# Optimization experiments

Hardware: AMD Instinct MI355X
Metric: run time of the kernel (lower is better)

The kernel has to match this reference:

```python
import jax, jax.numpy as jnp
import numpy as np

K = 16          # neighbors per query (args.k)
EPS_NORM = 1e-5  # LayerNorm / BatchNorm eps (torch default)


def _knn_edges(xyz, B, n):
    # batch-aware kNN: equal-sized batches, edges never cross batch boundary
    x = xyz.reshape(B, n, 3)
    d2 = jnp.sum((x[:, :, None, :] - x[:, None, :, :]) ** 2, -1)   # [B,n,n]
    _, idx = jax.lax.top_k(-d2, K)                                 # [B,n,K] local neighbor ids
    col = (idx + (jnp.arange(B) * n)[:, None, None]).reshape(-1)   # source (neighbor) [E]
    row = jnp.repeat(jnp.arange(B * n), K)                         # target (query)    [E]
    return row, col


def _forward(support_xyz, batch_index, features, lang_features, mask_flattened,
             W1, b1, ln_g, ln_b, W2, b2,
             Wl1, bl1, bn_g, bn_b, Wl2, bl2,
             Wr1, br1, Wr2, br2, row, col):
    N = support_xyz.shape[0]
    B, L, Fl = lang_features.shape
    # feat_encoder: Linear -> LayerNorm -> ReLU -> Linear
    h = features @ W1 + b1
    mu = h.mean(-1, keepdims=True)
    var = ((h - mu) ** 2).mean(-1, keepdims=True)
    h = (h - mu) / jnp.sqrt(var + EPS_NORM) * ln_g + ln_b
    feats = jax.nn.relu(h) @ W2 + b2                               # [N,F]
    # lang_encoder: Linear -> BatchNorm1d (batch statistics) -> ReLU -> Linear
    hl = lang_features.reshape(B * L, Fl) @ Wl1 + bl1
    mul = hl.mean(0)
    varl = ((hl - mul) ** 2).mean(0)
    hl = (hl - mul) / jnp.sqrt(varl + EPS_NORM) * bn_g + bn_b
    lang = (jax.nn.relu(hl) @ Wl2 + bl2).reshape(B, L, -1)         # [B,L,F]
    lang_flat = lang[batch_index]                                  # [N,L,F]
    # per-point / per-token attention logits
    atten = jnp.einsum('nf,nlf->nl', feats, lang_flat)             # [N,L]
    # segment softmax over incoming kNN edges (CenterOp max / add)
    attenmax = jax.ops.segment_max(atten[col], row, num_segments=N, indices_are_sorted=True)
    a = jnp.exp(atten[col] - attenmax[row])                        # [E,L]
    attensum = jax.ops.segment_sum(a, row, num_segments=N, indices_are_sorted=True)
    # CenterConv message
    att = a / attensum[row] * mask_flattened[row]                  # [E,L]
    att = att / (att.sum(-1, keepdims=True) + 1e-7)
    ctx = jnp.einsum('el,elf->ef', att, lang_flat[col])            # [E,F] attended lang feat
    xi, xj = support_xyz[row], support_xyz[col]
    d = xi - xj
    nrm = jnp.sqrt(jnp.sum(d * d, -1, keepdims=True) + 1e-12)
    ew = jnp.concatenate([xi, xj, d, nrm], -1)                     # [E,10]
    ew = jax.nn.relu(ew @ Wr1 + br1) @ Wr2 + br2                   # [E,F] rel_encoder
    msg = feats[col] * ctx * ew                                    # [E,F]
    rel = jax.ops.segment_sum(msg, row, num_segments=N, indices_are_sorted=True)
    return feats + rel


def setup_inputs() -> dict:
    key = jax.random.key(0)
    ks = jax.random.split(key, 12)
    B, n, L = 4, 1024, 16
    N = B * n
    Fv, Fl, F = 256, 768, 128
    def w(k, shp, fan):
        return jax.random.normal(k, shp, jnp.float32) / np.sqrt(fan).astype(np.float32)
    mask = (jax.random.uniform(ks[3], (N, L)) < 0.8).astype(jnp.float32).at[:, 0].set(1.0)
    return {
        'support_xyz': jax.random.normal(ks[0], (N, 3), jnp.float32),
        'batch_index': jnp.repeat(jnp.arange(B), n),
        'features': jax.random.normal(ks[1], (N, Fv), jnp.float32),
        'lang_features': jax.random.normal(ks[2], (B, L, Fl), jnp.float32),
        'mask_flattened': mask,
        'W1': w(ks[4], (Fv, F), Fv), 'b1': jnp.zeros(F, jnp.float32),
        'ln_g': jnp.ones(F, jnp.float32), 'ln_b': jnp.zeros(F, jnp.float32),
        'W2': w(ks[5], (F, F), F), 'b2': jnp.zeros(F, jnp.float32),
        'Wl1': w(ks[6], (Fl, F), Fl), 'bl1': jnp.zeros(F, jnp.float32),
        'bn_g': jnp.ones(F, jnp.float32), 'bn_b': jnp.zeros(F, jnp.float32),
        'Wl2': w(ks[7], (F, F), F), 'bl2': jnp.zeros(F, jnp.float32),
        'Wr1': w(ks[8], (10, 64), 10), 'br1': jnp.zeros(64, jnp.float32),
        'Wr2': w(ks[9], (64, F), 64), 'br2': jnp.zeros(F, jnp.float32),
    }


def reference(support_xyz, batch_index, features, lang_features, mask_flattened,
              W1, b1, ln_g, ln_b, W2, b2,
              Wl1, bl1, bn_g, bn_b, Wl2, bl2,
              Wr1, br1, Wr2, br2):
    B = lang_features.shape[0]
    n = support_xyz.shape[0] // B
    row, col = _knn_edges(support_xyz, B, n)
    return _forward(support_xyz, batch_index, features, lang_features, mask_flattened,
                    W1, b1, ln_g, ln_b, W2, b2,
                    Wl1, bl1, bn_g, bn_b, Wl2, bl2,
                    Wr1, br1, Wr2, br2, row, col)
```

## Files before the change

### kernel.cpp

```cpp
#include <hip/hip_runtime.h>

typedef unsigned long long u64;
typedef short short8 __attribute__((ext_vector_type(8)));
typedef float f32x4 __attribute__((ext_vector_type(4)));

#define N_PTS   4096
#define B_SZ    4
#define N_PER_B 1024
#define L_TOK   16
#define FV      256
#define FL      768
#define FDIM    128
#define KNN     16
#define RH      64

__device__ __forceinline__ short f2bf(float f) {
    unsigned int x = __float_as_uint(f);
    unsigned int r = (x + 0x7fffu + ((x >> 16) & 1u)) >> 16;
    return (short)r;
}

__global__ __launch_bounds__(256) void k1_kernel(const float* __restrict__ xyz,
                                                 const float* __restrict__ features,
                                                 const float* __restrict__ lf,
                                                 const float* __restrict__ W1,
                                                 const float* __restrict__ b1,
                                                 const float* __restrict__ ln_g,
                                                 const float* __restrict__ ln_b,
                                                 const float* __restrict__ W2,
                                                 const float* __restrict__ b2,
                                                 const float* __restrict__ Wl1,
                                                 const float* __restrict__ bl1,
                                                 int* __restrict__ knn,
                                                 float* __restrict__ feats,
                                                 float* __restrict__ hl) {
    __shared__ float smem[4 * 256 + 4 * 128 + 16];
    int b = blockIdx.x, t = threadIdx.x;

    if (b < 1024) {
        int lane = t & 63;
        int q = b * 4 + (t >> 6);
        int base = (q >> 10) << 10;
        float qx = xyz[q * 3 + 0];
        float qy = xyz[q * 3 + 1];
        float qz = xyz[q * 3 + 2];
        u64 keys[16];
#pragma unroll
        for (int m = 0; m < 16; m++) {
            int j = base + lane + (m << 6);
            float dx = qx - xyz[j * 3 + 0];
            float dy = qy - xyz[j * 3 + 1];
            float dz = qz - xyz[j * 3 + 2];
            float d2 = __fadd_rn(__fadd_rn(__fmul_rn(dx, dx), __fmul_rn(dy, dy)),
                                 __fmul_rn(dz, dz));
            keys[m] = (((u64)__float_as_uint(d2)) << 32) | (unsigned int)j;
        }
        for (int r = 0; r < KNN; r++) {
            u64 lmin = keys[0];
#pragma unroll
            for (int m = 1; m < 16; m++) lmin = (keys[m] < lmin) ? keys[m] : lmin;
            u64 g = lmin;
#pragma unroll
            for (int off = 32; off > 0; off >>= 1) {
                u64 o = __shfl_xor(g, off, 64);
                g = (o < g) ? o : g;
            }
#pragma unroll
            for (int m = 0; m < 16; m++)
                if (keys[m] == g) keys[m] = ~0ULL;
            if (lane == 0) knn[q * KNN + r] = (int)(g & 0xffffffffu);
        }
    } else if (b < 2048) {
        int i0 = (b - 1024) * 4;
        float* fin  = smem;
        float* rbuf = smem + 1024;
        float* red  = smem + 1536;
        for (int p = t; p < 4 * FV; p += 256) {
            int pp = p >> 8, k = p & 255;
            fin[pp * FV + k] = features[(i0 + pp) * FV + k];
        }
        __syncthreads();
        int c = t & 127, h = t >> 7;
        int p0 = 2 * h, p1 = 2 * h + 1;
        float bv = b1[c];
        float acc0 = bv, acc1 = bv;
        for (int k = 0; k < FV; k++) {
            float w = W1[k * FDIM + c];
            acc0 += fin[p0 * FV + k] * w;
            acc1 += fin[p1 * FV + k] * w;
        }
        float s0 = acc0, q0 = acc0 * acc0, s1 = acc1, q1 = acc1 * acc1;
#pragma unroll
        for (int off = 32; off > 0; off >>= 1) {
            s0 += __shfl_xor(s0, off, 64);
            q0 += __shfl_xor(q0, off, 64);
            s1 += __shfl_xor(s1, off, 64);
            q1 += __shfl_xor(q1, off, 64);
        }
        int wid = t >> 6;
        if ((t & 63) == 0) {
            red[wid * 4 + 0] = s0; red[wid * 4 + 1] = q0;
            red[wid * 4 + 2] = s1; red[wid * 4 + 3] = q1;
        }
        __syncthreads();
        float S0 = red[(2 * h) * 4 + 0] + red[(2 * h + 1) * 4 + 0];
        float Q0 = red[(2 * h) * 4 + 1] + red[(2 * h + 1) * 4 + 1];
        float S1 = red[(2 * h) * 4 + 2] + red[(2 * h + 1) * 4 + 2];
        float Q1 = red[(2 * h) * 4 + 3] + red[(2 * h + 1) * 4 + 3];
        float g = ln_g[c], bb = ln_b[c];
        float mu0 = S0 * (1.f / 128.f), var0 = Q0 * (1.f / 128.f) - mu0 * mu0;
        float mu1 = S1 * (1.f / 128.f), var1 = Q1 * (1.f / 128.f) - mu1 * mu1;
        float r0 = fmaxf((acc0 - mu0) * rsqrtf(var0 + 1e-5f) * g + bb, 0.f);
        float r1 = fmaxf((acc1 - mu1) * rsqrtf(var1 + 1e-5f) * g + bb, 0.f);
        rbuf[p0 * FDIM + c] = r0;
        rbuf[p1 * FDIM + c] = r1;
        __syncthreads();
        float b2v = b2[c];
        float f0 = b2v, f1 = b2v;
        for (int k = 0; k < FDIM; k++) {
            float w = W2[k * FDIM + c];
            f0 += rbuf[p0 * FDIM + k] * w;
            f1 += rbuf[p1 * FDIM + k] * w;
        }
        feats[(i0 + p0) * FDIM + c] = f0;
        feats[(i0 + p1) * FDIM + c] = f1;
    } else {
        int r = b - 2048;
        float* lrow = smem;
        float* part = smem + 768;
        for (int k = t; k < FL; k += 256) lrow[k] = lf[r * FL + k];
        __syncthreads();
        int c = t & 127, kh = t >> 7;
        float acc = (kh == 0) ? bl1[c] : 0.f;
        int k0 = kh * 384;
        for (int k = k0; k < k0 + 384; k++) acc += lrow[k] * Wl1[k * FDIM + c];
        part[kh * FDIM + c] = acc;
        __syncthreads();
        if (kh == 0) hl[r * FDIM + c] = part[c] + part[FDIM + c];
    }
}

__global__ __launch_bounds__(128) void lang2_kernel(const float* __restrict__ hl,
                                                    const float* __restrict__ bn_g,
                                                    const float* __restrict__ bn_b,
                                                    const float* __restrict__ Wl2,
                                                    const float* __restrict__ bl2,
                                                    float* __restrict__ lang) {
    __shared__ float rl4[4][FDIM];
    int t = threadIdx.x;
    int r0 = blockIdx.x * 4;
    float s = 0.f, s2 = 0.f;
    for (int r = 0; r < 64; r++) {
        float v = hl[r * FDIM + t];
        s += v; s2 += v * v;
    }
    float mu = s * (1.f / 64.f);
    float var = s2 * (1.f / 64.f) - mu * mu;
    float rs = rsqrtf(var + 1e-5f);
    float g = bn_g[t], bb = bn_b[t];
#pragma unroll
    for (int p = 0; p < 4; p++)
        rl4[p][t] = fmaxf((hl[(r0 + p) * FDIM + t] - mu) * rs * g + bb, 0.f);
    __syncthreads();
    float bv = bl2[t];
    float a0 = bv, a1 = bv, a2 = bv, a3 = bv;
    for (int k = 0; k < FDIM; k++) {
        float w = Wl2[k * FDIM + t];
        a0 += rl4[0][k] * w;
        a1 += rl4[1][k] * w;
        a2 += rl4[2][k] * w;
        a3 += rl4[3][k] * w;
    }
    lang[(r0 + 0) * FDIM + t] = a0;
    lang[(r0 + 1) * FDIM + t] = a1;
    lang[(r0 + 2) * FDIM + t] = a2;
    lang[(r0 + 3) * FDIM + t] = a3;
}

__global__ __launch_bounds__(256) void atten_kernel(const float* __restrict__ feats,
                                                    const float* __restrict__ lang,
                                                    float* __restrict__ atten) {
    __shared__ float fb[2][FDIM];
    __shared__ float pb[256];
    int t = threadIdx.x;
    int half = t >> 7, tt = t & 127;
    int i = blockIdx.x * 2 + half;
    fb[half][tt] = feats[i * FDIM + tt];
    __syncthreads();
    int l = tt >> 3, sj = tt & 7;
    int bi = i >> 10;
    const float* lrow = lang + (bi * L_TOK + l) * FDIM;
    float p = 0.f;
#pragma unroll
    for (int m = 0; m < 16; m++) {
        int k = sj + (m << 3);
        p += fb[half][k] * lrow[k];
    }
    pb[t] = p;
    __syncthreads();
    if (tt < L_TOK) {
        float a = 0.f;
#pragma unroll
        for (int u = 0; u < 8; u++) a += pb[half * 128 + tt * 8 + u];
        atten[i * L_TOK + tt] = a;
    }
}

__global__ __launch_bounds__(256) void edge_kernel(const float* __restrict__ xyz,
                                                   const float* __restrict__ mask,
                                                   const float* __restrict__ Wr1,
                                                   const float* __restrict__ br1,
                                                   const float* __restrict__ Wr2,
                                                   const float* __restrict__ br2,
                                                   const int* __restrict__ knn,
                                                   const float* __restrict__ lang,
                                                   const float* __restrict__ feats,
                                                   const float* __restrict__ atten,
                                                   float* __restrict__ out) {
    int lane = threadIdx.x & 63;
    int wid  = threadIdx.x >> 6;
    int i    = blockIdx.x * 4 + wid;
    int bi   = i >> 10;
    int quad = lane >> 4;
    int e16  = lane & 15;

    int idxe = knn[i * KNN + e16];

    float sat[8];
    if (quad < 2) {
        const float4* ap = (const float4*)(atten + idxe * L_TOK + quad * 8);
        float4 a0 = ap[0], a1 = ap[1];
        sat[0] = a0.x; sat[1] = a0.y; sat[2] = a0.z; sat[3] = a0.w;
        sat[4] = a1.x; sat[5] = a1.y; sat[6] = a1.z; sat[7] = a1.w;
    } else {
#pragma unroll
        for (int j = 0; j < 8; j++) sat[j] = 0.f;
    }

    float mx[8];
#pragma unroll
    for (int j = 0; j < 8; j++) mx[j] = sat[j];
#pragma unroll
    for (int off = 1; off < 16; off <<= 1) {
#pragma unroll
        for (int j = 0; j < 8; j++) mx[j] = fmaxf(mx[j], __shfl_xor(mx[j], off, 16));
    }
    float ex[8], sm[8];
#pragma unroll
    for (int j = 0; j < 8; j++) { ex[j] = __expf(sat[j] - mx[j]); sm[j] = ex[j]; }
#pragma unroll
    for (int off = 1; off < 16; off <<= 1) {
#pragma unroll
        for (int j = 0; j < 8; j++) sm[j] += __shfl_xor(sm[j], off, 16);
    }
    float st[8];
    if (quad < 2) {
        const float4* mp = (const float4*)(mask + i * L_TOK + quad * 8);
        float4 m0 = mp[0], m1 = mp[1];
        float mv[8] = {m0.x, m0.y, m0.z, m0.w, m1.x, m1.y, m1.z, m1.w};
#pragma unroll
        for (int j = 0; j < 8; j++) st[j] = ex[j] * (mv[j] / sm[j]);
    } else {
#pragma unroll
        for (int j = 0; j < 8; j++) st[j] = 0.f;
    }
    float s = st[0] + st[1] + st[2] + st[3] + st[4] + st[5] + st[6] + st[7];
    s += __shfl_xor(s, 16, 64);
    s += __shfl_xor(s, 32, 64);
    float inv2 = 1.f / (s + 1e-7f);
    short8 sattA;
#pragma unroll
    for (int j = 0; j < 8; j++) sattA[j] = f2bf(st[j] * inv2);

    float xi0 = xyz[i * 3 + 0], xi1 = xyz[i * 3 + 1], xi2 = xyz[i * 3 + 2];
    float xj0 = xyz[idxe * 3 + 0], xj1 = xyz[idxe * 3 + 1], xj2 = xyz[idxe * 3 + 2];
    float d0 = xi0 - xj0, d1 = xi1 - xj1, d2v = xi2 - xj2;
    float nr = sqrtf(d0 * d0 + d1 * d1 + d2v * d2v + 1e-12f);
    float ein[10] = {xi0, xi1, xi2, xj0, xj1, xj2, d0, d1, d2v, nr};
    short8 hidA[2];
#pragma unroll
    for (int sstep = 0; sstep < 2; sstep++) {
        int k0 = sstep * 32 + quad * 8;
        float h[8];
        const float4* bp = (const float4*)(br1 + k0);
        float4 b0 = bp[0], b1v = bp[1];
        h[0] = b0.x; h[1] = b0.y; h[2] = b0.z; h[3] = b0.w;
        h[4] = b1v.x; h[5] = b1v.y; h[6] = b1v.z; h[7] = b1v.w;
#pragma unroll
        for (int m = 0; m < 10; m++) {
            const float4* wp = (const float4*)(Wr1 + m * RH + k0);
            float4 w0 = wp[0], w1 = wp[1];
            float em = ein[m];
            h[0] += em * w0.x; h[1] += em * w0.y; h[2] += em * w0.z; h[3] += em * w0.w;
            h[4] += em * w1.x; h[5] += em * w1.y; h[6] += em * w1.z; h[7] += em * w1.w;
        }
#pragma unroll
        for (int j = 0; j < 8; j++) hidA[sstep][j] = f2bf(fmaxf(h[j], 0.f));
    }

    int idxr[4];
#pragma unroll
    for (int r = 0; r < 4; r++) idxr[r] = knn[i * KNN + quad * 4 + r];

#pragma unroll 2
    for (int tile = 0; tile < 8; tile++) {
        int cc = tile * 16 + e16;
        f32x4 accew = {0.f, 0.f, 0.f, 0.f};
#pragma unroll
        for (int sstep = 0; sstep < 2; sstep++) {
            short8 w2B;
#pragma unroll
            for (int j = 0; j < 8; j++)
                w2B[j] = f2bf(Wr2[(sstep * 32 + quad * 8 + j) * FDIM + cc]);
            accew = __builtin_amdgcn_mfma_f32_16x16x32_bf16(hidA[sstep], w2B, accew, 0, 0, 0);
        }
        short8 lsB;
        if (quad < 2) {
#pragma unroll
            for (int j = 0; j < 8; j++)
                lsB[j] = f2bf(lang[bi * L_TOK * FDIM + (quad * 8 + j) * FDIM + cc]);
        } else {
#pragma unroll
            for (int j = 0; j < 8; j++) lsB[j] = 0;
        }
        f32x4 accctx = {0.f, 0.f, 0.f, 0.f};
        accctx = __builtin_amdgcn_mfma_f32_16x16x32_bf16(sattA, lsB, accctx, 0, 0, 0);

        float br2c = br2[cc];
        float msum = 0.f;
#pragma unroll
        for (int r = 0; r < 4; r++) {
            float fj = feats[idxr[r] * FDIM + cc];
            msum += fj * accctx[r] * (accew[r] + br2c);
        }
        msum += __shfl_xor(msum, 16, 64);
        msum += __shfl_xor(msum, 32, 64);
        if (lane < 16)
            out[i * FDIM + cc] = feats[i * FDIM + cc] + msum;
    }
}

extern "C" void kernel_launch(void* const* d_in, const int* in_sizes, int n_in,
                              void* d_out, int out_size, void* d_ws, size_t ws_size,
                              hipStream_t stream) {
    const float* xyz   = (const float*)d_in[0];
    const float* features = (const float*)d_in[2];
    const float* lang_f   = (const float*)d_in[3];
    const float* mask     = (const float*)d_in[4];
    const float* W1   = (const float*)d_in[5];
    const float* b1   = (const float*)d_in[6];
    const float* ln_g = (const float*)d_in[7];
    const float* ln_b = (const float*)d_in[8];
    const float* W2   = (const float*)d_in[9];
    const float* b2   = (const float*)d_in[10];
    const float* Wl1  = (const float*)d_in[11];
    const float* bl1  = (const float*)d_in[12];
    const float* bn_g = (const float*)d_in[13];
    const float* bn_b = (const float*)d_in[14];
    const float* Wl2  = (const float*)d_in[15];
    const float* bl2  = (const float*)d_in[16];
    const float* Wr1  = (const float*)d_in[17];
    const float* br1  = (const float*)d_in[18];
    const float* Wr2  = (const float*)d_in[19];
    const float* br2  = (const float*)d_in[20];

    float* ws_feats = (float*)d_ws;
    float* ws_atten = ws_feats + N_PTS * FDIM;
    float* ws_lang  = ws_atten + N_PTS * L_TOK;
    float* ws_hl    = ws_lang + B_SZ * L_TOK * FDIM;
    int*   ws_knn   = (int*)(ws_hl + 64 * FDIM);

    k1_kernel<<<2112, 256, 0, stream>>>(xyz, features, lang_f,
                                        W1, b1, ln_g, ln_b, W2, b2,
                                        Wl1, bl1, ws_knn, ws_feats, ws_hl);
    lang2_kernel<<<16, 128, 0, stream>>>(ws_hl, bn_g, bn_b, Wl2, bl2, ws_lang);
    atten_kernel<<<N_PTS / 2, 256, 0, stream>>>(ws_feats, ws_lang, ws_atten);
    edge_kernel<<<N_PTS / 4, 256, 0, stream>>>(xyz, mask, Wr1, br1, Wr2, br2,
                                               ws_knn, ws_lang, ws_feats, ws_atten,
                                               (float*)d_out);
}
```

Measured before the change: 166.0 us.

## Compute feat encoder with split-bf16 MFMA and fuse lang BN stage into new kernel

Result: no change. 164.1 us (-1.1%).

```diff
diff --git a/kernel.cpp b/kernel.cpp
--- a/kernel.cpp
+++ b/kernel.cpp
@@ -1,8 +1,10 @@
 #include <hip/hip_runtime.h>
 
 typedef unsigned long long u64;
+typedef unsigned int u32;
 typedef short short8 __attribute__((ext_vector_type(8)));
 typedef float f32x4 __attribute__((ext_vector_type(4)));
+typedef u32 u32x4v __attribute__((ext_vector_type(4)));
 
 #define N_PTS   4096
 #define B_SZ    4
@@ -14,6 +16,8 @@
 #define KNN     16
 #define RH      64
 
+#define MFMA_BF16(a, b, c) __builtin_amdgcn_mfma_f32_16x16x32_bf16((a), (b), (c), 0, 0, 0)
+
 __device__ __forceinline__ short f2bf(float f) {
     unsigned int x = __float_as_uint(f);
     unsigned int r = (x + 0x7fffu + ((x >> 16) & 1u)) >> 16;
@@ -23,18 +27,19 @@
 __global__ __launch_bounds__(256) void k1_kernel(const float* __restrict__ xyz,
                                                  const float* __restrict__ features,
                                                  const float* __restrict__ lf,
-                                                 const float* __restrict__ W1,
-                                                 const float* __restrict__ b1,
-                                                 const float* __restrict__ ln_g,
-                                                 const float* __restrict__ ln_b,
-                                                 const float* __restrict__ W2,
-                                                 const float* __restrict__ b2,
                                                  const float* __restrict__ Wl1,
                                                  const float* __restrict__ bl1,
+                                                 const float* __restrict__ W1,
+                                                 const float* __restrict__ W2,
                                                  int* __restrict__ knn,
-                                                 float* __restrict__ feats,
-                                                 float* __restrict__ hl) {
-    __shared__ float smem[4 * 256 + 4 * 128 + 16];
+                                                 float* __restrict__ hl,
+                                                 short* __restrict__ fp_hi,
+                                                 short* __restrict__ fp_lo,
+                                                 short* __restrict__ w1p_hi,
+                                                 short* __restrict__ w1p_lo,
+                                                 short* __restrict__ w2p_hi,
+                                                 short* __restrict__ w2p_lo) {
+    __shared__ float smem[1024];
     int b = blockIdx.x, t = threadIdx.x;
 
     if (b < 1024) {
@@ -70,62 +75,8 @@
                 if (keys[m] == g) keys[m] = ~0ULL;
             if (lane == 0) knn[q * KNN + r] = (int)(g & 0xffffffffu);
         }
-    } else if (b < 2048) {
-        int i0 = (b - 1024) * 4;
-        float* fin  = smem;
-        float* rbuf = smem + 1024;
-        float* red  = smem + 1536;
-        for (int p = t; p < 4 * FV; p += 256) {
-            int pp = p >> 8, k = p & 255;
-            fin[pp * FV + k] = features[(i0 + pp) * FV + k];
-        }
-        __syncthreads();
-        int c = t & 127, h = t >> 7;
-        int p0 = 2 * h, p1 = 2 * h + 1;
-        float bv = b1[c];
-        float acc0 = bv, acc1 = bv;
-        for (int k = 0; k < FV; k++) {
-            float w = W1[k * FDIM + c];
-            acc0 += fin[p0 * FV + k] * w;
-            acc1 += fin[p1 * FV + k] * w;
-        }
-        float s0 = acc0, q0 = acc0 * acc0, s1 = acc1, q1 = acc1 * acc1;
-#pragma unroll
-        for (int off = 32; off > 0; off >>= 1) {
-            s0 += __shfl_xor(s0, off, 64);
-            q0 += __shfl_xor(q0, off, 64);
-            s1 += __shfl_xor(s1, off, 64);
-            q1 += __shfl_xor(q1, off, 64);
-        }
-        int wid = t >> 6;
-        if ((t & 63) == 0) {
-            red[wid * 4 + 0] = s0; red[wid * 4 + 1] = q0;
-            red[wid * 4 + 2] = s1; red[wid * 4 + 3] = q1;
-        }
-        __syncthreads();
-        float S0 = red[(2 * h) * 4 + 0] + red[(2 * h + 1) * 4 + 0];
-        float Q0 = red[(2 * h) * 4 + 1] + red[(2 * h + 1) * 4 + 1];
-        float S1 = red[(2 * h) * 4 + 2] + red[(2 * h + 1) * 4 + 2];
-        float Q1 = red[(2 * h) * 4 + 3] + red[(2 * h + 1) * 4 + 3];
-        float g = ln_g[c], bb = ln_b[c];
-        float mu0 = S0 * (1.f / 128.f), var0 = Q0 * (1.f / 128.f) - mu0 * mu0;
-        float mu1 = S1 * (1.f / 128.f), var1 = Q1 * (1.f / 128.f) - mu1 * mu1;
-        float r0 = fmaxf((acc0 - mu0) * rsqrtf(var0 + 1e-5f) * g + bb, 0.f);
-        float r1 = fmaxf((acc1 - mu1) * rsqrtf(var1 + 1e-5f) * g + bb, 0.f);
-        rbuf[p0 * FDIM + c] = r0;
-        rbuf[p1 * FDIM + c] = r1;
-        __syncthreads();
-        float b2v = b2[c];
-        float f0 = b2v, f1 = b2v;
-        for (int k = 0; k < FDIM; k++) {
-            float w = W2[k * FDIM + c];
-            f0 += rbuf[p0 * FDIM + k] * w;
-            f1 += rbuf[p1 * FDIM + k] * w;
-        }
-        feats[(i0 + p0) * FDIM + c] = f0;
-        feats[(i0 + p1) * FDIM + c] = f1;
-    } else {
-        int r = b - 2048;
+    } else if (b < 1088) {
+        int r = b - 1024;
         float* lrow = smem;
         float* part = smem + 768;
         for (int k = t; k < FL; k += 256) lrow[k] = lf[r * FL + k];
@@ -137,44 +88,205 @@
         part[kh * FDIM + c] = acc;
         __syncthreads();
         if (kh == 0) hl[r * FDIM + c] = part[c] + part[FDIM + c];
+    } else if (b < 1344) {
+        int rt = b - 1088;
+        int lane = t & 63, kh = t >> 6;
+        int e = lane & 15, q = lane >> 4;
+#pragma unroll
+        for (int pp = 0; pp < 2; pp++) {
+            int ks = kh * 2 + pp;
+            const float* src = features + (rt * 16 + e) * FV + ks * 32 + q * 8;
+            float4 f0 = *(const float4*)src;
+            float4 f1 = *(const float4*)(src + 4);
+            float f[8] = {f0.x, f0.y, f0.z, f0.w, f1.x, f1.y, f1.z, f1.w};
+            short8 hi, lo;
+#pragma unroll
+            for (int j = 0; j < 8; j++) {
+                u32 bits = __float_as_uint(f[j]);
+                hi[j] = (short)(bits >> 16);
+                float lof = f[j] - __uint_as_float(bits & 0xffff0000u);
+                lo[j] = (short)(__float_as_uint(lof) >> 16);
+            }
+            int o = ((rt * 8 + ks) * 64 + lane) * 8;
+            *(short8*)(fp_hi + o) = hi;
+            *(short8*)(fp_lo + o) = lo;
+        }
+    } else {
+        int isW2 = (b >= 1352);
+        int ks = isW2 ? (b - 1352) : (b - 1344);
+        const float* W = isW2 ? W2 : W1;
+        short* ph = isW2 ? w2p_hi : w1p_hi;
+        short* pl = isW2 ? w2p_lo : w1p_lo;
+        int lane = t & 63, cth = t >> 6;
+        int e = lane & 15, q = lane >> 4;
+#pragma unroll
+        for (int p = 0; p < 2; p++) {
+            int ct = cth * 2 + p;
+            short8 hi, lo;
+#pragma unroll
+            for (int j = 0; j < 8; j++) {
+                float w = W[(ks * 32 + q * 8 + j) * FDIM + ct * 16 + e];
+                u32 bits = __float_as_uint(w);
+                hi[j] = (short)(bits >> 16);
+                float lof = w - __uint_as_float(bits & 0xffff0000u);
+                lo[j] = (short)(__float_as_uint(lof) >> 16);
+            }
+            int o = ((ks * 8 + ct) * 64 + lane) * 8;
+            *(short8*)(ph + o) = hi;
+            *(short8*)(pl + o) = lo;
+        }
     }
 }
 
-__global__ __launch_bounds__(128) void lang2_kernel(const float* __restrict__ hl,
-                                                    const float* __restrict__ bn_g,
-                                                    const float* __restrict__ bn_b,
-                                                    const float* __restrict__ Wl2,
-                                                    const float* __restrict__ bl2,
-                                                    float* __restrict__ lang) {
-    __shared__ float rl4[4][FDIM];
-    int t = threadIdx.x;
-    int r0 = blockIdx.x * 4;
-    float s = 0.f, s2 = 0.f;
-    for (int r = 0; r < 64; r++) {
-        float v = hl[r * FDIM + t];
-        s += v; s2 += v * v;
-    }
-    float mu = s * (1.f / 64.f);
-    float var = s2 * (1.f / 64.f) - mu * mu;
-    float rs = rsqrtf(var + 1e-5f);
-    float g = bn_g[t], bb = bn_b[t];
-#pragma unroll
-    for (int p = 0; p < 4; p++)
-        rl4[p][t] = fmaxf((hl[(r0 + p) * FDIM + t] - mu) * rs * g + bb, 0.f);
-    __syncthreads();
-    float bv = bl2[t];
-    float a0 = bv, a1 = bv, a2 = bv, a3 = bv;
-    for (int k = 0; k < FDIM; k++) {
-        float w = Wl2[k * FDIM + t];
-        a0 += rl4[0][k] * w;
-        a1 += rl4[1][k] * w;
-        a2 += rl4[2][k] * w;
-        a3 += rl4[3][k] * w;
-    }
-    lang[(r0 + 0) * FDIM + t] = a0;
-    lang[(r0 + 1) * FDIM + t] = a1;
-    lang[(r0 + 2) * FDIM + t] = a2;
-    lang[(r0 + 3) * FDIM + t] = a3;
+__global__ __launch_bounds__(256) void k2_kernel(const short* __restrict__ fp_hi,
+                                                 const short* __restrict__ fp_lo,
+                                                 const short* __restrict__ w1p_hi,
+                                                 const short* __restrict__ w1p_lo,
+                                                 const short* __restrict__ w2p_hi,
+                                                 const short* __restrict__ w2p_lo,
+                                                 const float* __restrict__ b1,
+                                                 const float* __restrict__ ln_g,
+                                                 const float* __restrict__ ln_b,
+                                                 const float* __restrict__ b2,
+                                                 const float* __restrict__ hl,
+                                                 const float* __restrict__ bn_g,
+                                                 const float* __restrict__ bn_b,
+                                                 const float* __restrict__ Wl2,
+                                                 const float* __restrict__ bl2,
+                                                 float* __restrict__ feats,
+                                                 float* __restrict__ lang) {
+    int b = blockIdx.x, t = threadIdx.x;
+    if (b < 64) {
+        __shared__ u32 hbuf[4][16 * 132];
+        int wid = t >> 6, lane = t & 63;
+        int e = lane & 15, q = lane >> 4;
+        int rt = b * 4 + wid;
+
+        f32x4 acc[8];
+#pragma unroll
+        for (int ct = 0; ct < 8; ct++) {
+            float v = b1[ct * 16 + e];
+            acc[ct] = (f32x4){v, v, v, v};
+        }
+        for (int ks = 0; ks < 8; ks++) {
+            int ao = ((rt * 8 + ks) * 64 + lane) * 8;
+            short8 ah = *(const short8*)(fp_hi + ao);
+            short8 al = *(const short8*)(fp_lo + ao);
+#pragma unroll
+            for (int ct = 0; ct < 8; ct++) {
+                int bo = ((ks * 8 + ct) * 64 + lane) * 8;
+                short8 bh = *(const short8*)(w1p_hi + bo);
+                short8 bl = *(const short8*)(w1p_lo + bo);
+                acc[ct] = MFMA_BF16(ah, bh, acc[ct]);
+                acc[ct] = MFMA_BF16(al, bh, acc[ct]);
+                acc[ct] = MFMA_BF16(ah, bl, acc[ct]);
+            }
+        }
+        float s[4], sq[4];
+#pragma unroll
+        for (int r = 0; r < 4; r++) { s[r] = 0.f; sq[r] = 0.f; }
+#pragma unroll
+        for (int ct = 0; ct < 8; ct++)
+#pragma unroll
+            for (int r = 0; r < 4; r++) {
+                float v = acc[ct][r];
+                s[r] += v; sq[r] += v * v;
+            }
+#pragma unroll
+        for (int off = 1; off < 16; off <<= 1)
+#pragma unroll
+            for (int r = 0; r < 4; r++) {
+                s[r] += __shfl_xor(s[r], off, 16);
+                sq[r] += __shfl_xor(sq[r], off, 16);
+            }
+        float mu[4], rs[4];
+#pragma unroll
+        for (int r = 0; r < 4; r++) {
+            mu[r] = s[r] * (1.f / 128.f);
+            float var = sq[r] * (1.f / 128.f) - mu[r] * mu[r];
+            rs[r] = rsqrtf(var + 1e-5f);
+        }
+        u32* hrow = &hbuf[wid][0];
+#pragma unroll
+        for (int ct = 0; ct < 8; ct++) {
+            float g = ln_g[ct * 16 + e], bb = ln_b[ct * 16 + e];
+#pragma unroll
+            for (int r = 0; r < 4; r++) {
+                float n = fmaxf((acc[ct][r] - mu[r]) * rs[r] * g + bb, 0.f);
+                u32 nb = __float_as_uint(n);
+                u32 hh = nb & 0xffff0000u;
+                float lof = n - __uint_as_float(hh);
+                hrow[(q * 4 + r) * 132 + ct * 16 + e] = hh | (__float_as_uint(lof) >> 16);
+            }
+        }
+        f32x4 acc2[8];
+#pragma unroll
+        for (int ct = 0; ct < 8; ct++) {
+            float v = b2[ct * 16 + e];
+            acc2[ct] = (f32x4){v, v, v, v};
+        }
+#pragma unroll
+        for (int ks = 0; ks < 4; ks++) {
+            u32 hv[8];
+            *(u32x4v*)&hv[0] = *(const u32x4v*)&hrow[e * 132 + ks * 32 + q * 8];
+            *(u32x4v*)&hv[4] = *(const u32x4v*)&hrow[e * 132 + ks * 32 + q * 8 + 4];
+            short8 ah, al;
+#pragma unroll
+            for (int j = 0; j < 8; j++) {
+                ah[j] = (short)(hv[j] >> 16);
+                al[j] = (short)(hv[j] & 0xffffu);
+            }
+#pragma unroll
+            for (int ct = 0; ct < 8; ct++) {
+                int bo = ((ks * 8 + ct) * 64 + lane) * 8;
+                short8 bh = *(const short8*)(w2p_hi + bo);
+                short8 bl = *(const short8*)(w2p_lo + bo);
+                acc2[ct] = MFMA_BF16(ah, bh, acc2[ct]);
+                acc2[ct] = MFMA_BF16(al, bh, acc2[ct]);
+                acc2[ct] = MFMA_BF16(ah, bl, acc2[ct]);
+            }
+        }
+#pragma unroll
+        for (int ct = 0; ct < 8; ct++)
+#pragma unroll
+            for (int r = 0; r < 4; r++)
+                feats[(rt * 16 + q * 4 + r) * FDIM + ct * 16 + e] = acc2[ct][r];
+    } else {
+        __shared__ float rl4[4][FDIM];
+        int tt = t & 127;
+        int act = (t < 128);
+        int r0 = (b - 64) * 4;
+        if (act) {
+            float s = 0.f, s2 = 0.f;
+            for (int r = 0; r < 64; r++) {
+                float v = hl[r * FDIM + tt];
+                s += v; s2 += v * v;
+            }
+            float mu = s * (1.f / 64.f);
+            float var = s2 * (1.f / 64.f) - mu * mu;
+            float rs = rsqrtf(var + 1e-5f);
+            float g = bn_g[tt], bb = bn_b[tt];
+#pragma unroll
+            for (int p = 0; p < 4; p++)
+                rl4[p][tt] = fmaxf((hl[(r0 + p) * FDIM + tt] - mu) * rs * g + bb, 0.f);
+        }
+        __syncthreads();
+        if (act) {
+            float bv = bl2[tt];
+            float a0 = bv, a1 = bv, a2 = bv, a3 = bv;
+            for (int k = 0; k < FDIM; k++) {
+                float w = Wl2[k * FDIM + tt];
+                a0 += rl4[0][k] * w;
+                a1 += rl4[1][k] * w;
+                a2 += rl4[2][k] * w;
+                a3 += rl4[3][k] * w;
+            }
+            lang[(r0 + 0) * FDIM + tt] = a0;
+            lang[(r0 + 1) * FDIM + tt] = a1;
+            lang[(r0 + 2) * FDIM + tt] = a2;
+            lang[(r0 + 3) * FDIM + tt] = a3;
+        }
+    }
 }
 
 __global__ __launch_bounds__(256) void atten_kernel(const float* __restrict__ feats,
@@ -369,11 +481,20 @@
     float* ws_lang  = ws_atten + N_PTS * L_TOK;
     float* ws_hl    = ws_lang + B_SZ * L_TOK * FDIM;
     int*   ws_knn   = (int*)(ws_hl + 64 * FDIM);
-
-    k1_kernel<<<2112, 256, 0, stream>>>(xyz, features, lang_f,
-                                        W1, b1, ln_g, ln_b, W2, b2,
-                                        Wl1, bl1, ws_knn, ws_feats, ws_hl);
-    lang2_kernel<<<16, 128, 0, stream>>>(ws_hl, bn_g, bn_b, Wl2, bl2, ws_lang);
+    short* fp_hi    = (short*)(ws_knn + N_PTS * KNN);
+    short* fp_lo    = fp_hi + N_PTS * FV;
+    short* w1p_hi   = fp_lo + N_PTS * FV;
+    short* w1p_lo   = w1p_hi + FV * FDIM;
+    short* w2p_hi   = w1p_lo + FV * FDIM;
+    short* w2p_lo   = w2p_hi + FDIM * FDIM;
+
+    k1_kernel<<<1356, 256, 0, stream>>>(xyz, features, lang_f, Wl1, bl1, W1, W2,
+                                        ws_knn, ws_hl,
+                                        fp_hi, fp_lo, w1p_hi, w1p_lo, w2p_hi, w2p_lo);
+    k2_kernel<<<80, 256, 0, stream>>>(fp_hi, fp_lo, w1p_hi, w1p_lo, w2p_hi, w2p_lo,
+                                      b1, ln_g, ln_b, b2,
+                                      ws_hl, bn_g, bn_b, Wl2, bl2,
+                                      ws_feats, ws_lang);
     atten_kernel<<<N_PTS / 2, 256, 0, stream>>>(ws_feats, ws_lang, ws_atten);
     edge_kernel<<<N_PTS / 4, 256, 0, stream>>>(xyz, mask, Wr1, br1, Wr2, br2,
                                                ws_knn, ws_lang, ws_feats, ws_atten,
```
